# Optimization experiments

Hardware: AMD Instinct MI355X
Metric: run time of the kernel (lower is better)

The kernel has to match this reference:

```python
import jax, jax.numpy as jnp
import numpy as np

N0, N1, N2, N3 = 8192, 32768, 65536, 65536
CUM = (N0, N0 + N1, N0 + N1 + N2, N0 + N1 + N2 + N3)  # nodes through hop k
NTOT = CUM[3]
EH = (131072, 262144, 262144)                          # edges per hop (per edge type)
ECUM = (EH[0], EH[0] + EH[1], EH[0] + EH[1] + EH[2])
ETOT = ECUM[2]
C, H, T = 64, 256, 3
HH = H // 2
B, L = 16, 512  # N0 == B * L: equal-length note sequences per graph
LN_EPS = 1e-5


def _ln(x, w, b):
    m = x.mean(-1, keepdims=True)
    v = x.var(-1, keepdims=True)
    return (x - m) / jnp.sqrt(v + LN_EPS) * w + b


def _seg_mean(msgs, dst, n):
    s = jax.ops.segment_sum(msgs, dst, num_segments=n)
    cnt = jax.ops.segment_sum(jnp.ones(dst.shape, msgs.dtype), dst, num_segments=n)
    return s / jnp.maximum(cnt, 1.0)[:, None]


def _l2(x):
    return x / jnp.maximum(jnp.linalg.norm(x, axis=-1, keepdims=True), 1e-12)


def _gru_dir(x, wih, whh, bih, bhh, reverse):
    # x: [B, Lt, Din]; torch gate order (r, z, n)
    gi = jnp.einsum('bld,gd->blg', x, wih) + bih
    gi = jnp.moveaxis(gi, 1, 0)  # [Lt, B, 3*HH]
    h0 = jnp.zeros((x.shape[0], HH), x.dtype)

    def step(h, g):
        gh = h @ whh.T + bhh
        ir, iz, in_ = jnp.split(g, 3, -1)
        hr, hz, hn = jnp.split(gh, 3, -1)
        r = jax.nn.sigmoid(ir + hr)
        z = jax.nn.sigmoid(iz + hz)
        n = jnp.tanh(in_ + r * hn)
        hnew = (1.0 - z) * n + z * h
        return hnew, hnew

    _, ys = jax.lax.scan(step, h0, gi, reverse=reverse)
    return jnp.moveaxis(ys, 0, 1)  # [B, Lt, HH]


def _bigru(x, wih, whh, bih, bhh):
    f = _gru_dir(x, wih[0], whh[0], bih[0], bhh[0], False)
    bwd = _gru_dir(x, wih[1], whh[1], bih[1], bhh[1], True)
    return jnp.concatenate([f, bwd], -1)


def _forward(x, edge_index, batch_size, sage0_proj_w, sage0_proj_b, sage0_lw, sage0_lb,
             sage0_rw, sage_lw, sage_lb, sage_rw, ln_w, ln_b,
             gru_wih0, gru_whh0, gru_bih0, gru_bhh0,
             gru_wih1, gru_whh1, gru_bih1, gru_bhh1,
             rnn_norm_w, rnn_norm_b, mlp1_w, mlp1_b, mlp_ln_w, mlp_ln_b,
             mlp2_w, mlp2_b, cat_w, cat_b):
    # ---- hybrid GRU branch on seed notes (equal lengths -> pad == reshape) ----
    xs = x[:batch_size].reshape(B, L, C)
    h = _bigru(xs, gru_wih0, gru_whh0, gru_bih0, gru_bhh0)
    h = _bigru(h, gru_wih1, gru_whh1, gru_bih1, gru_bhh1)  # inter-layer dropout: eval mode
    h = _ln(h, rnn_norm_w, rnn_norm_b)
    h = _ln(jax.nn.relu(h @ mlp1_w + mlp1_b), mlp_ln_w, mlp_ln_b) @ mlp2_w + mlp2_b
    x_rnn = h.reshape(batch_size, H)

    # ---- GNN layer 0: SAGEConv(project=True, normalize=True), hetero mean over T types ----
    feat = x
    outs = []
    for t in range(T):
        src, dst = edge_index[t, 0], edge_index[t, 1]
        xp = jax.nn.relu(feat @ sage0_proj_w[t] + sage0_proj_b[t])
        agg = _seg_mean(xp[src], dst, NTOT)
        outs.append(_l2(agg @ sage0_lw[t] + sage0_lb[t] + feat @ sage0_rw[t]))
    feat = sum(outs) / T
    feat = _ln(jax.nn.relu(feat), ln_w[0], ln_b[0])  # dropout: eval mode (identity)

    # ---- layers 1..2 with trim_to_layer: drop last sampled hop each layer ----
    n_layer = (CUM[2], CUM[1])
    e_layer = (ECUM[1], ECUM[0])
    for i in range(2):
        n, e = n_layer[i], e_layer[i]
        feat = feat[:n]
        outs = []
        for t in range(T):
            src, dst = edge_index[t, 0, :e], edge_index[t, 1, :e]
            agg = _seg_mean(feat[src], dst, n)
            outs.append(agg @ sage_lw[i, t] + sage_lb[i, t] + feat @ sage_rw[i, t])
        feat = sum(outs) / T
        if i == 0:
            feat = _ln(jax.nn.relu(feat), ln_w[1], ln_b[1])
    x_gnn = feat[:batch_size]
    return jnp.concatenate([x_rnn, x_gnn], -1) @ cat_w + cat_b


def setup_inputs():
    key = jax.random.key(0)
    ks = iter(jax.random.split(key, 64))

    def nrm(shape, fan_in):
        return jax.random.normal(next(ks), shape, jnp.float32) / float(np.sqrt(fan_in))

    # hop-structured edges: hop k has src < CUM[k+1], dst < CUM[k]
    ei = []
    for t in range(T):
        rows, cols = [], []
        for k in range(3):
            rows.append(jax.random.randint(next(ks), (EH[k],), 0, CUM[k + 1]))
            cols.append(jax.random.randint(next(ks), (EH[k],), 0, CUM[k]))
        ei.append(jnp.stack([jnp.concatenate(rows), jnp.concatenate(cols)]))
    edge_index = jnp.stack(ei).astype(jnp.int32)

    return dict(
        x=jax.random.normal(next(ks), (NTOT, C), jnp.float32),
        edge_index=edge_index,
        batch=(jnp.arange(N0) // L).astype(jnp.int32),
        batch_size=N0,
        sage0_proj_w=nrm((T, C, C), C), sage0_proj_b=jnp.zeros((T, C), jnp.float32),
        sage0_lw=nrm((T, C, H), C), sage0_lb=jnp.zeros((T, H), jnp.float32),
        sage0_rw=nrm((T, C, H), C),
        sage_lw=nrm((2, T, H, H), H), sage_lb=jnp.zeros((2, T, H), jnp.float32),
        sage_rw=nrm((2, T, H, H), H),
        ln_w=jnp.ones((2, H), jnp.float32), ln_b=jnp.zeros((2, H), jnp.float32),
        gru_wih0=nrm((2, 3 * HH, C), C), gru_whh0=nrm((2, 3 * HH, HH), HH),
        gru_bih0=jnp.zeros((2, 3 * HH), jnp.float32), gru_bhh0=jnp.zeros((2, 3 * HH), jnp.float32),
        gru_wih1=nrm((2, 3 * HH, H), H), gru_whh1=nrm((2, 3 * HH, HH), HH),
        gru_bih1=jnp.zeros((2, 3 * HH), jnp.float32), gru_bhh1=jnp.zeros((2, 3 * HH), jnp.float32),
        rnn_norm_w=jnp.ones((H,), jnp.float32), rnn_norm_b=jnp.zeros((H,), jnp.float32),
        mlp1_w=nrm((H, H), H), mlp1_b=jnp.zeros((H,), jnp.float32),
        mlp_ln_w=jnp.ones((H,), jnp.float32), mlp_ln_b=jnp.zeros((H,), jnp.float32),
        mlp2_w=nrm((H, H), H), mlp2_b=jnp.zeros((H,), jnp.float32),
        cat_w=nrm((2 * H, H), 2 * H), cat_b=jnp.zeros((H,), jnp.float32),
    )


def reference(x, edge_index, batch, batch_size, sage0_proj_w, sage0_proj_b, sage0_lw,
              sage0_lb, sage0_rw, sage_lw, sage_lb, sage_rw, ln_w, ln_b,
              gru_wih0, gru_whh0, gru_bih0, gru_bhh0, gru_wih1, gru_whh1, gru_bih1,
              gru_bhh1, rnn_norm_w, rnn_norm_b, mlp1_w, mlp1_b, mlp_ln_w, mlp_ln_b,
              mlp2_w, mlp2_b, cat_w, cat_b):
    # batch encodes 16 equal-length (512) sequences; bincount/pad == reshape above
    return _forward(x, edge_index, batch_size, sage0_proj_w, sage0_proj_b, sage0_lw,
                    sage0_lb, sage0_rw, sage_lw, sage_lb, sage_rw, ln_w, ln_b,
                    gru_wih0, gru_whh0, gru_bih0, gru_bhh0, gru_wih1, gru_whh1,
                    gru_bih1, gru_bhh1, rnn_norm_w, rnn_norm_b, mlp1_w, mlp1_b,
                    mlp_ln_w, mlp_ln_b, mlp2_w, mlp2_b, cat_w, cat_b)
```

## Files before the change

kernel.cpp:

```cpp
#include <hip/hip_runtime.h>
#include <stdint.h>

typedef unsigned short u16;
typedef __attribute__((ext_vector_type(8))) short short8;
typedef __attribute__((ext_vector_type(4))) short short4v;
typedef __attribute__((ext_vector_type(4))) float float4v;

#define DEV static __device__ __forceinline__

DEV float bf2f(u16 u){ union { unsigned int i; float f; } c; c.i = ((unsigned int)u) << 16; return c.f; }
DEV u16 f2bf(float f){ union { float ff; unsigned int i; } c; c.ff = f;
  unsigned int x = c.i; return (u16)((x + 0x7fffu + ((x >> 16) & 1u)) >> 16); }

#define MFMA16(a,b,c) __builtin_amdgcn_mfma_f32_16x16x32_bf16((a),(b),(c),0,0,0)

#define ETOTC  655360
#define TSTRIDE 155648
#define NBINS   466944

struct SM {
  u16 As[64*72];
  u16 Bs[256*72];
  float redS[4][64];
  float redQ[4][64];
  float rowA[64], rowB[64];
};

__global__ void detect_dtype(const u16* __restrict__ xs, int* __restrict__ flag){
  __shared__ int sh[256];
  int t = threadIdx.x; int cnt = 0;
  for (int i = t; i < 4096; i += 256){
    u16 u = xs[i]; int e = (u >> 7) & 0xff;
    cnt += (u == 0 || (e >= 112 && e <= 143)) ? 1 : 0;
  }
  sh[t] = cnt; __syncthreads();
  for (int d = 128; d; d >>= 1){ if (t < d) sh[t] += sh[t+d]; __syncthreads(); }
  if (t == 0) flag[0] = (sh[0] >= 3686) ? 1 : 0;
}

DEV u16 scrub(u16 v){ int e = (v >> 7) & 0xff; return (e == 0xff) ? (u16)0 : v; }

__global__ void convert_x(const void* __restrict__ xin, const int* __restrict__ flag,
                          u16* __restrict__ out){
  int i = blockIdx.x*256 + threadIdx.x;
  u16 v[4];
  if (flag[0] == 1){
    short4v s = ((const short4v*)xin)[i];
#pragma unroll
    for (int j=0;j<4;j++) v[j] = scrub((u16)s[j]);
  } else {
    float4v f = ((const float4v*)xin)[i];
#pragma unroll
    for (int j=0;j<4;j++) v[j] = scrub(f2bf(f[j]));
  }
  short4v o; o[0]=(short)v[0]; o[1]=(short)v[1]; o[2]=(short)v[2]; o[3]=(short)v[3];
  ((short4v*)out)[i] = o;
}

struct WSrc { const void* p[28]; };
__device__ const int g_wcum[29] = {0,12288,12480,61632,62400,111552,504768,506304,899520,
  900032,900544,949696,1048000,1048768,1049536,1246144,1344448,1345216,1345984,1346240,
  1346496,1412032,1412288,1412544,1412800,1478336,1478592,1609664,1609920};

__global__ void convert_w(WSrc d, const int* __restrict__ flag, u16* __restrict__ out){
  int i = blockIdx.x*256 + threadIdx.x;
  if (i >= 1609920) return;
  int lo = 0, hi = 28;
  while (hi - lo > 1){ int m = (lo+hi) >> 1; if (i >= g_wcum[m]) lo = m; else hi = m; }
  int off = i - g_wcum[lo];
  u16 v = (flag[0] == 1) ? ((const u16*)d.p[lo])[off]
                         : f2bf(((const float*)d.p[lo])[off]);
  out[i] = scrub(v);
}

__global__ void packT(const u16* __restrict__ in, u16* __restrict__ out, int K, int N){
  int i = blockIdx.x*256 + threadIdx.x;
  if (i < K*N){ int n = i / K, k = i - n*K; out[i] = in[(size_t)k*N + n]; }
}

__global__ void pack_lr(const u16* __restrict__ lw, const u16* __restrict__ rw,
                        u16* __restrict__ out, int F){
  int K2 = 2*F; long total = 3L*256*K2;
  long i = (long)blockIdx.x*256 + threadIdx.x;
  if (i < total){
    int k = (int)(i % K2); int n = (int)((i / K2) & 255); int t = (int)(i / ((long)K2*256));
    out[i] = (k < F) ? lw[((size_t)t*F + k)*256 + n]
                     : rw[((size_t)t*F + (k-F))*256 + n];
  }
}

__global__ void hist3(const int* __restrict__ ei, int* __restrict__ cnt){
  int g = blockIdx.x*256 + threadIdx.x;
  int t = g / ETOTC, e = g - t*ETOTC;
  int dst = ei[(size_t)t*2*ETOTC + ETOTC + e];
  int base = t*TSTRIDE;
  atomicAdd(&cnt[base + dst], 1);
  if (e < 393216) atomicAdd(&cnt[base + 106496 + dst], 1);
  if (e < 131072) atomicAdd(&cnt[base + 147456 + dst], 1);
}

__global__ void perm3(const int* __restrict__ ei, const int* __restrict__ off,
                      int* __restrict__ slot, int* __restrict__ srcs){
  int g = blockIdx.x*256 + threadIdx.x;
  int t = g / ETOTC, e = g - t*ETOTC;
  int dst = ei[(size_t)t*2*ETOTC + ETOTC + e];
  int src = ei[(size_t)t*2*ETOTC + e];
  int base = t*TSTRIDE;
  { int b = base + dst; srcs[off[b] + atomicAdd(&slot[b], 1)] = src; }
  if (e < 393216){ int b = base + 106496 + dst;
    srcs[off[b] + atomicAdd(&slot[b], 1)] = src; }
  if (e < 131072){ int b = base + 147456 + dst;
    srcs[off[b] + atomicAdd(&slot[b], 1)] = src; }
}

__global__ void scan_blocks(const int* __restrict__ cnt, int* __restrict__ off,
                            int* __restrict__ bsum, int n){
  __shared__ int sh[256];
  int t = threadIdx.x;
  int base = blockIdx.x*2048 + t*8;
  int v[8]; int tot = 0;
#pragma unroll
  for (int j=0;j<8;j++){ v[j] = (base+j < n) ? cnt[base+j] : 0; tot += v[j]; }
  sh[t] = tot; __syncthreads();
  for (int d=1; d<256; d<<=1){
    int y = (t>=d) ? sh[t-d] : 0; __syncthreads();
    sh[t] += y; __syncthreads();
  }
  int run = sh[t] - tot;
#pragma unroll
  for (int j=0;j<8;j++){ if (base+j < n) off[base+j] = run; run += v[j]; }
  if (t == 255) bsum[blockIdx.x] = sh[255];
}

__global__ void scan_top(int* __restrict__ bsum, int G){
  __shared__ int sh[256];
  int t = threadIdx.x;
  int v = (t < G) ? bsum[t] : 0;
  sh[t] = v; __syncthreads();
  for (int d=1; d<256; d<<=1){
    int y = (t>=d) ? sh[t-d] : 0; __syncthreads();
    sh[t] += y; __syncthreads();
  }
  if (t < G) bsum[t] = sh[t] - v;
}

__global__ void scan_add(int* __restrict__ off, const int* __restrict__ bsum, int n){
  int add = bsum[blockIdx.x];
  int base = blockIdx.x*2048 + threadIdx.x*8;
#pragma unroll
  for (int j=0;j<8;j++) if (base+j < n) off[base+j] += add;
}

template<int F>
DEV void gather_body(int w, int lane,
    const int* __restrict__ off, const int* __restrict__ cnt, const int* __restrict__ srcs,
    const u16* __restrict__ feat, int ld, u16* __restrict__ out)
{
  int st = off[w], c = cnt[w];
  float sc = 1.f / (float)(c < 1 ? 1 : c);
  if (F == 64) {
    float a = 0.f, b = 0.f;
    int i = 0;
    for (; i + 4 <= c; i += 4){
      int s0 = srcs[st+i], s1 = srcs[st+i+1], s2 = srcs[st+i+2], s3 = srcs[st+i+3];
      u16 u0 = feat[(size_t)s0*ld + lane];
      u16 u1 = feat[(size_t)s1*ld + lane];
      u16 u2 = feat[(size_t)s2*ld + lane];
      u16 u3 = feat[(size_t)s3*ld + lane];
      a += bf2f(u0) + bf2f(u1);
      b += bf2f(u2) + bf2f(u3);
    }
    for (; i < c; ++i){ int s = srcs[st+i]; a += bf2f(feat[(size_t)s*ld + lane]); }
    out[(size_t)w*64 + lane] = f2bf((a + b)*sc);
  } else {
    float a0=0.f,a1=0.f,a2=0.f,a3=0.f;
    float b0=0.f,b1=0.f,b2=0.f,b3=0.f;
    int i = 0;
    for (; i + 4 <= c; i += 4){
      int s0 = srcs[st+i], s1 = srcs[st+i+1], s2 = srcs[st+i+2], s3 = srcs[st+i+3];
      short4v u0 = *(const short4v*)(feat + (size_t)s0*ld + lane*4);
      short4v u1 = *(const short4v*)(feat + (size_t)s1*ld + lane*4);
      short4v u2 = *(const short4v*)(feat + (size_t)s2*ld + lane*4);
      short4v u3 = *(const short4v*)(feat + (size_t)s3*ld + lane*4);
      a0 += bf2f((u16)u0[0]) + bf2f((u16)u1[0]);
      a1 += bf2f((u16)u0[1]) + bf2f((u16)u1[1]);
      a2 += bf2f((u16)u0[2]) + bf2f((u16)u1[2]);
      a3 += bf2f((u16)u0[3]) + bf2f((u16)u1[3]);
      b0 += bf2f((u16)u2[0]) + bf2f((u16)u3[0]);
      b1 += bf2f((u16)u2[1]) + bf2f((u16)u3[1]);
      b2 += bf2f((u16)u2[2]) + bf2f((u16)u3[2]);
      b3 += bf2f((u16)u2[3]) + bf2f((u16)u3[3]);
    }
    for (; i < c; ++i){
      int s = srcs[st+i];
      short4v u = *(const short4v*)(feat + (size_t)s*ld + lane*4);
      a0 += bf2f((u16)u[0]); a1 += bf2f((u16)u[1]);
      a2 += bf2f((u16)u[2]); a3 += bf2f((u16)u[3]);
    }
    u16* o = out + (size_t)w*256 + lane*4;
    o[0]=f2bf((a0+b0)*sc); o[1]=f2bf((a1+b1)*sc);
    o[2]=f2bf((a2+b2)*sc); o[3]=f2bf((a3+b3)*sc);
  }
}

DEV void ln_body(int r, int lane,
    const u16* __restrict__ in, u16* __restrict__ out,
    const u16* __restrict__ w, const u16* __restrict__ b)
{
  short4v u = *(const short4v*)(in + (size_t)r*256 + lane*4);
  float v[4];
#pragma unroll
  for (int i=0;i<4;i++) v[i] = bf2f((u16)u[i]);
  float s = v[0]+v[1]+v[2]+v[3];
  float q = v[0]*v[0]+v[1]*v[1]+v[2]*v[2]+v[3]*v[3];
#pragma unroll
  for (int d=1; d<64; d<<=1){ s += __shfl_xor(s, d); q += __shfl_xor(q, d); }
  float mu = s * (1.f/256.f);
  float var = fmaxf(q * (1.f/256.f) - mu*mu, 0.f);
  float rs = rsqrtf(var + 1e-5f);
  u16* o = out + (size_t)r*256 + lane*4;
#pragma unroll
  for (int i=0;i<4;i++){
    int col = lane*4 + i;
    o[i] = f2bf((v[i]-mu)*rs*bf2f(w[col]) + bf2f(b[col]));
  }
}

#define LGKM0_SB do{ asm volatile("s_waitcnt lgkmcnt(0)" ::: "memory"); \
                     __builtin_amdgcn_sched_barrier(0); \
                     __builtin_amdgcn_s_barrier(); \
                     __builtin_amdgcn_sched_barrier(0); }while(0)

#define GRU_STEP(S, C0, C1, C2) do{                                          \
    const int l_ = dir ? (511 - (S)) : (S);                                  \
    short8 afr_[4];                                                          \
    _Pragma("unroll")                                                        \
    for (int kt=0; kt<4; kt++) afr_[kt] = *(const short8*)(&hbf[kt*32 + lg*8]); \
    float4v acc_[4];                                                         \
    _Pragma("unroll")                                                        \
    for (int nt=0; nt<4; nt++) acc_[nt] = (float4v){0.f,0.f,0.f,0.f};        \
    _Pragma("unroll")                                                        \
    for (int kt=0; kt<4; kt++){                                              \
      _Pragma("unroll")                                                      \
      for (int nt=0; nt<4; nt++) acc_[nt] = MFMA16(afr_[kt], bfrag[nt][kt], acc_[nt]); } \
    if (lane < 16){                                                          \
      _Pragma("unroll")                                                      \
      for (int nt=0; nt<4; nt++) ghs[64*w + nt*16 + lane] = acc_[nt][0];     \
    }                                                                        \
    LGKM0_SB;                                                                \
    if (tid < 128){                                                          \
      float ghr = ghs[tid]       + bhr;                                      \
      float ghz = ghs[128 + tid] + bhz;                                      \
      float ghn = ghs[256 + tid] + bhn;                                      \
      float r_ = 1.f/(1.f + __expf(-((C0) + ghr)));                          \
      float z_ = 1.f/(1.f + __expf(-((C1) + ghz)));                          \
      float xn_ = (C2) + r_*ghn;                                             \
      float th_ = 1.f - 2.f/(__expf(2.f*xn_) + 1.f);                         \
      hreg = (1.f - z_)*th_ + z_*hreg;                                       \
      u16 hb_ = f2bf(hreg);                                                  \
      hbf[tid] = hb_;                                                        \
      hout[((size_t)(b*512 + l_))*256 + dir*128 + tid] = hb_;                \
      int sn_ = (S) + 2;                                                     \
      if (sn_ < 512){                                                        \
        int ln2_ = dir ? (511 - sn_) : sn_;                                  \
        const float* g_ = gbase + (size_t)ln2_*768;                          \
        (C0) = g_[0]; (C1) = g_[128]; (C2) = g_[256];                        \
      }                                                                      \
    }                                                                        \
    LGKM0_SB;                                                                \
  }while(0)

DEV void gru_body(const float* __restrict__ gi, const u16* __restrict__ whh,
                  const u16* __restrict__ bhh, u16* __restrict__ hout,
                  int bid, u16* hbf, float* ghs)
{
  const int b = bid >> 1, dir = bid & 1;
  const int tid = threadIdx.x;
  const int w = tid >> 6, lane = tid & 63;
  const int lr = lane & 15, lg = lane >> 4;

  short8 bfrag[4][4];
#pragma unroll
  for (int nt=0; nt<4; nt++)
#pragma unroll
    for (int kt=0; kt<4; kt++){
      int n = 64*w + nt*16 + lr;
      bfrag[nt][kt] = *(const short8*)(whh + ((size_t)(dir*384 + n))*128 + kt*32 + lg*8);
    }

  const float* gbase = gi + (size_t)b*512*768 + dir*384 + tid;
  float hreg = 0.f, bhr = 0.f, bhz = 0.f, bhn = 0.f;
  float a0=0.f,a1=0.f,a2=0.f, e0=0.f,e1=0.f,e2=0.f;
  if (tid < 128){
    bhr = bf2f(bhh[dir*384 + tid]);
    bhz = bf2f(bhh[dir*384 + 128 + tid]);
    bhn = bf2f(bhh[dir*384 + 256 + tid]);
    const float* g0 = gbase + (size_t)(dir ? 511 : 0)*768;
    a0 = g0[0]; a1 = g0[128]; a2 = g0[256];
    const float* g1 = gbase + (size_t)(dir ? 510 : 1)*768;
    e0 = g1[0]; e1 = g1[128]; e2 = g1[256];
  }
  if (tid < 64) ((unsigned int*)hbf)[tid] = 0u;
  LGKM0_SB;

  __builtin_amdgcn_s_setprio(1);
  for (int s2 = 0; s2 < 512; s2 += 2){
    GRU_STEP(s2,     a0, a1, a2);
    GRU_STEP(s2 + 1, e0, e1, e2);
  }
  __builtin_amdgcn_s_setprio(0);
}

template<int F>
__global__ __launch_bounds__(384,1) void fused_gru_gather(
    const float* __restrict__ gi, const u16* __restrict__ whh,
    const u16* __restrict__ bhh, u16* __restrict__ hout,
    const int* __restrict__ off0, const int* __restrict__ cnt0, const int* __restrict__ srcs,
    const u16* __restrict__ feat, int ld, int featstep,
    u16* __restrict__ aggout, long aggstride, int rows, int bpt)
{
  __shared__ u16 hbf[128];
  __shared__ float ghs[384];
  if (blockIdx.x < 32){
    gru_body(gi, whh, bhh, hout, blockIdx.x, hbf, ghs);
    return;
  }
  int gb = blockIdx.x - 32;
  int t = gb / bpt, rb = gb - t*bpt;
  int w = rb*6 + (threadIdx.x >> 6);
  int lane = threadIdx.x & 63;
  if (w >= rows) return;
  gather_body<F>(w, lane, off0 + t*TSTRIDE, cnt0 + t*TSTRIDE, srcs,
                 feat + (size_t)t*featstep, ld, aggout + (size_t)t*aggstride);
}

template<int EPI, bool OUTF32>
DEV void gemm_body(SM& sm, int bx, int by,
    const u16* __restrict__ A, int lda,
    const u16* __restrict__ WT, int K, int N,
    const u16* __restrict__ bias,
    const u16* __restrict__ lnw, const u16* __restrict__ lnb,
    void* __restrict__ Cp, int ldc, const int* __restrict__ dynof)
{
  u16* As = sm.As; u16* Bs = sm.Bs;
  const int tid = threadIdx.x;
  const int lane = tid & 63, wid = tid >> 6;
  const int lr = lane & 15, lg = lane >> 4;
  const int m0 = bx * 64;
  const int col0 = by * 256;
  float4v acc[4][4];
#pragma unroll
  for (int i=0;i<4;i++)
#pragma unroll
    for (int j=0;j<4;j++) acc[i][j] = (float4v){0.f,0.f,0.f,0.f};

  for (int k0 = 0; k0 < K; k0 += 64){
#pragma unroll
    for (int v = 0; v < 2; v++){
      int idx = tid + v*256; int r = idx >> 3, c8 = (idx & 7) << 3;
      *(short8*)(&As[r*72 + c8]) = *(const short8*)(A + (size_t)(m0+r)*lda + k0 + c8);
    }
#pragma unroll
    for (int v = 0; v < 8; v++){
      int idx = tid + v*256; int nn = idx >> 3, c8 = (idx & 7) << 3;
      short8 val = {0,0,0,0,0,0,0,0};
      if (col0 + nn < N) val = *(const short8*)(WT + (size_t)(col0+nn)*K + k0 + c8);
      *(short8*)(&Bs[nn*72 + c8]) = val;
    }
    __syncthreads();
#pragma unroll
    for (int kk = 0; kk < 2; kk++){
      short8 af[4], bfr[4];
#pragma unroll
      for (int i=0;i<4;i++) af[i]  = *(const short8*)(&As[(16*i+lr)*72 + kk*32 + lg*8]);
#pragma unroll
      for (int j=0;j<4;j++) bfr[j] = *(const short8*)(&Bs[(wid*64+16*j+lr)*72 + kk*32 + lg*8]);
#pragma unroll
      for (int i=0;i<4;i++)
#pragma unroll
        for (int j=0;j<4;j++) acc[i][j] = MFMA16(af[i], bfr[j], acc[i][j]);
    }
    __syncthreads();
  }
  int cols[4];
#pragma unroll
  for (int j=0;j<4;j++) cols[j] = col0 + wid*64 + 16*j + lr;
#pragma unroll
  for (int j=0;j<4;j++){
    float bv = (cols[j] < N) ? bf2f(bias[cols[j]]) : 0.f;
#pragma unroll
    for (int i=0;i<4;i++)
#pragma unroll
      for (int r=0;r<4;r++) acc[i][j][r] += bv;
  }
  if (EPI >= 1){
#pragma unroll
    for (int i=0;i<4;i++)
#pragma unroll
      for (int j=0;j<4;j++)
#pragma unroll
        for (int r=0;r<4;r++) acc[i][j][r] = fmaxf(acc[i][j][r], 0.f);
  }
  if (EPI == 2){
#pragma unroll
    for (int i=0;i<4;i++)
#pragma unroll
      for (int r=0;r<4;r++){
        float p = acc[i][0][r]+acc[i][1][r]+acc[i][2][r]+acc[i][3][r];
        float q = acc[i][0][r]*acc[i][0][r]+acc[i][1][r]*acc[i][1][r]
                 +acc[i][2][r]*acc[i][2][r]+acc[i][3][r]*acc[i][3][r];
#pragma unroll
        for (int d=1; d<16; d<<=1){ p += __shfl_xor(p,d); q += __shfl_xor(q,d); }
        if (lr == 0){ sm.redS[wid][16*i + lg*4 + r] = p; sm.redQ[wid][16*i + lg*4 + r] = q; }
      }
    __syncthreads();
    if (tid < 64){
      float s = sm.redS[0][tid]+sm.redS[1][tid]+sm.redS[2][tid]+sm.redS[3][tid];
      float q = sm.redQ[0][tid]+sm.redQ[1][tid]+sm.redQ[2][tid]+sm.redQ[3][tid];
      float mu = s * (1.f/256.f);
      float var = fmaxf(q * (1.f/256.f) - mu*mu, 0.f);
      sm.rowA[tid] = mu; sm.rowB[tid] = rsqrtf(var + 1e-5f);
    }
    __syncthreads();
#pragma unroll
    for (int i=0;i<4;i++)
#pragma unroll
      for (int r=0;r<4;r++){
        int rl = 16*i + lg*4 + r;
        float mu = sm.rowA[rl], rs = sm.rowB[rl];
#pragma unroll
        for (int j=0;j<4;j++){
          float w = bf2f(lnw[cols[j]]), bb = bf2f(lnb[cols[j]]);
          acc[i][j][r] = (acc[i][j][r]-mu)*rs*w + bb;
        }
      }
  }
  bool of32 = OUTF32;
  if (dynof) of32 = (dynof[0] == 0);
#pragma unroll
  for (int i=0;i<4;i++)
#pragma unroll
    for (int r=0;r<4;r++){
      int row = m0 + 16*i + lg*4 + r;
#pragma unroll
      for (int j=0;j<4;j++) if (cols[j] < N){
        if (of32) ((float*)Cp)[(size_t)row*ldc + cols[j]] = acc[i][j][r];
        else ((u16*)Cp)[(size_t)row*ldc + cols[j]] = f2bf(acc[i][j][r]);
      }
    }
}

template<int EPI, bool OUTF32>
__global__ __launch_bounds__(256,1) void gemm_bt(
    const u16* __restrict__ A, int lda,
    const u16* __restrict__ WT, int K, int N,
    const u16* __restrict__ bias,
    const u16* __restrict__ lnw, const u16* __restrict__ lnb,
    void* __restrict__ Cp, int ldc, const int* __restrict__ dynof)
{
  __shared__ SM sm;
  gemm_body<EPI,OUTF32>(sm, blockIdx.x, blockIdx.y, A, lda, WT, K, N, bias, lnw, lnb, Cp, ldc, dynof);
}

template<int F, bool DO_L2, bool DO_LN>
DEV void sage_body(SM& sm, int bx,
    const u16* __restrict__ A1, long a1t, const u16* __restrict__ A2, int lda2,
    const u16* __restrict__ WTp, const u16* __restrict__ lbp,
    const u16* __restrict__ lnw, const u16* __restrict__ lnb,
    u16* __restrict__ out, int ldc, int outcol)
{
  constexpr int K2 = 2*F;
  u16* As = sm.As; u16* Bs = sm.Bs;
  const int tid = threadIdx.x;
  const int lane = tid & 63, wid = tid >> 6;
  const int lr = lane & 15, lg = lane >> 4;
  const int m0 = bx * 64;
  int colsL[4];
#pragma unroll
  for (int j=0;j<4;j++) colsL[j] = wid*64 + 16*j + lr;
  float4v facc[4][4];
#pragma unroll
  for (int i=0;i<4;i++)
#pragma unroll
    for (int j=0;j<4;j++) facc[i][j] = (float4v){0.f,0.f,0.f,0.f};

  for (int t=0; t<3; ++t){
    float4v acc[4][4];
#pragma unroll
    for (int i=0;i<4;i++)
#pragma unroll
      for (int j=0;j<4;j++) acc[i][j] = (float4v){0.f,0.f,0.f,0.f};
    const u16* WT  = WTp + (size_t)t*256*K2;
    const u16* A1b = A1 + (size_t)t*a1t;
    for (int k0 = 0; k0 < K2; k0 += 64){
      const u16* Ab; int la, kb;
      if (k0 < F){ Ab = A1b; la = F; kb = k0; } else { Ab = A2; la = lda2; kb = k0 - F; }
#pragma unroll
      for (int v=0; v<2; v++){
        int idx = tid + v*256; int r = idx >> 3, c8 = (idx & 7) << 3;
        *(short8*)(&As[r*72 + c8]) = *(const short8*)(Ab + (size_t)(m0+r)*la + kb + c8);
      }
#pragma unroll
      for (int v=0; v<8; v++){
        int idx = tid + v*256; int nn = idx >> 3, c8 = (idx & 7) << 3;
        *(short8*)(&Bs[nn*72 + c8]) = *(const short8*)(WT + (size_t)nn*K2 + k0 + c8);
      }
      __syncthreads();
#pragma unroll
      for (int kk = 0; kk < 2; kk++){
        short8 af[4], bfr[4];
#pragma unroll
        for (int i=0;i<4;i++) af[i]  = *(const short8*)(&As[(16*i+lr)*72 + kk*32 + lg*8]);
#pragma unroll
        for (int j=0;j<4;j++) bfr[j] = *(const short8*)(&Bs[(wid*64+16*j+lr)*72 + kk*32 + lg*8]);
#pragma unroll
        for (int i=0;i<4;i++)
#pragma unroll
          for (int j=0;j<4;j++) acc[i][j] = MFMA16(af[i], bfr[j], acc[i][j]);
      }
      __syncthreads();
    }
#pragma unroll
    for (int j=0;j<4;j++){
      float bv = bf2f(lbp[t*256 + colsL[j]]);
#pragma unroll
      for (int i=0;i<4;i++)
#pragma unroll
        for (int r=0;r<4;r++) acc[i][j][r] += bv;
    }
    if (DO_L2){
#pragma unroll
      for (int i=0;i<4;i++)
#pragma unroll
        for (int r=0;r<4;r++){
          float q = acc[i][0][r]*acc[i][0][r]+acc[i][1][r]*acc[i][1][r]
                   +acc[i][2][r]*acc[i][2][r]+acc[i][3][r]*acc[i][3][r];
#pragma unroll
          for (int d=1; d<16; d<<=1) q += __shfl_xor(q,d);
          if (lr == 0) sm.redQ[wid][16*i + lg*4 + r] = q;
        }
      __syncthreads();
      if (tid < 64){
        float q = sm.redQ[0][tid]+sm.redQ[1][tid]+sm.redQ[2][tid]+sm.redQ[3][tid];
        sm.rowA[tid] = 1.f / fmaxf(sqrtf(q), 1e-12f);
      }
      __syncthreads();
#pragma unroll
      for (int i=0;i<4;i++)
#pragma unroll
        for (int r=0;r<4;r++){
          float sc = sm.rowA[16*i + lg*4 + r];
#pragma unroll
          for (int j=0;j<4;j++) acc[i][j][r] *= sc;
        }
      __syncthreads();
    }
#pragma unroll
    for (int i=0;i<4;i++)
#pragma unroll
      for (int j=0;j<4;j++)
#pragma unroll
        for (int r=0;r<4;r++) facc[i][j][r] += acc[i][j][r];
  }
  const float inv3 = (1.f/3.f);
#pragma unroll
  for (int i=0;i<4;i++)
#pragma unroll
    for (int j=0;j<4;j++)
#pragma unroll
      for (int r=0;r<4;r++) facc[i][j][r] *= inv3;
  if (DO_LN){
#pragma unroll
    for (int i=0;i<4;i++)
#pragma unroll
      for (int j=0;j<4;j++)
#pragma unroll
        for (int r=0;r<4;r++) facc[i][j][r] = fmaxf(facc[i][j][r], 0.f);
#pragma unroll
    for (int i=0;i<4;i++)
#pragma unroll
      for (int r=0;r<4;r++){
        float p = facc[i][0][r]+facc[i][1][r]+facc[i][2][r]+facc[i][3][r];
        float q = facc[i][0][r]*facc[i][0][r]+facc[i][1][r]*facc[i][1][r]
                 +facc[i][2][r]*facc[i][2][r]+facc[i][3][r]*facc[i][3][r];
#pragma unroll
        for (int d=1; d<16; d<<=1){ p += __shfl_xor(p,d); q += __shfl_xor(q,d); }
        if (lr == 0){ sm.redS[wid][16*i + lg*4 + r] = p; sm.redQ[wid][16*i + lg*4 + r] = q; }
      }
    __syncthreads();
    if (tid < 64){
      float s = sm.redS[0][tid]+sm.redS[1][tid]+sm.redS[2][tid]+sm.redS[3][tid];
      float q = sm.redQ[0][tid]+sm.redQ[1][tid]+sm.redQ[2][tid]+sm.redQ[3][tid];
      float mu = s * (1.f/256.f);
      float var = fmaxf(q * (1.f/256.f) - mu*mu, 0.f);
      sm.rowA[tid] = mu; sm.rowB[tid] = rsqrtf(var + 1e-5f);
    }
    __syncthreads();
#pragma unroll
    for (int i=0;i<4;i++)
#pragma unroll
      for (int r=0;r<4;r++){
        int rl = 16*i + lg*4 + r;
        float mu = sm.rowA[rl], rs = sm.rowB[rl];
#pragma unroll
        for (int j=0;j<4;j++){
          float w = bf2f(lnw[colsL[j]]), bb = bf2f(lnb[colsL[j]]);
          facc[i][j][r] = (facc[i][j][r]-mu)*rs*w + bb;
        }
      }
  }
#pragma unroll
  for (int i=0;i<4;i++)
#pragma unroll
    for (int r=0;r<4;r++){
      int row = m0 + 16*i + lg*4 + r;
#pragma unroll
      for (int j=0;j<4;j++)
        out[(size_t)row*ldc + outcol + colsL[j]] = f2bf(facc[i][j][r]);
    }
}

__global__ __launch_bounds__(256,1) void fused_gemm_sage0(
    const u16* __restrict__ H0, const u16* __restrict__ wih1b, const u16* __restrict__ bih1b,
    float* __restrict__ GI,
    const u16* __restrict__ AGGB0, const u16* __restrict__ x16, const u16* __restrict__ WP0,
    const u16* __restrict__ s0lb, const u16* __restrict__ lnw, const u16* __restrict__ lnb,
    u16* __restrict__ FEAT)
{
  __shared__ SM sm;
  int b = blockIdx.x;
  if (b < 384)
    gemm_body<0,true>(sm, b & 127, b >> 7, H0, 256, wih1b, 256, 768, bih1b,
                      nullptr, nullptr, GI, 768, nullptr);
  else
    sage_body<64,true,true>(sm, b - 384, AGGB0, (long)106496*64, x16, 64, WP0, s0lb,
                            lnw, lnb, FEAT, 256, 0);
}

__global__ __launch_bounds__(256,1) void fused_ln_sage1(
    const u16* __restrict__ AGGB1, const u16* __restrict__ FEAT, const u16* __restrict__ WP1,
    const u16* __restrict__ slb, const u16* __restrict__ lnw, const u16* __restrict__ lnb,
    u16* __restrict__ FEAT2,
    const u16* __restrict__ H1, u16* __restrict__ HA,
    const u16* __restrict__ rnw, const u16* __restrict__ rnb)
{
  __shared__ SM sm;
  int b = blockIdx.x;
  if (b < 640)
    sage_body<256,false,true>(sm, b, AGGB1, (long)40960*256, FEAT, 256, WP1, slb,
                              lnw, lnb, FEAT2, 256, 0);
  else {
    int r = (b - 640)*4 + (threadIdx.x >> 6);
    ln_body(r, threadIdx.x & 63, H1, HA, rnw, rnb);
  }
}

__global__ __launch_bounds__(256,1) void fused_mlp1_gather2(
    const u16* __restrict__ HA, const u16* __restrict__ M1T, const u16* __restrict__ mlp1b,
    const u16* __restrict__ mlnw, const u16* __restrict__ mlnb, u16* __restrict__ HB,
    const int* __restrict__ OFF, const int* __restrict__ CNT, const int* __restrict__ SRCS,
    const u16* __restrict__ FEAT2, u16* __restrict__ AGGB2)
{
  __shared__ SM sm;
  int b = blockIdx.x;
  if (b < 128){
    gemm_body<2,false>(sm, b, 0, HA, 256, M1T, 256, 256, mlp1b, mlnw, mlnb, HB, 256, nullptr);
  } else {
    int g = b - 128;
    int t = g / 2048, rb = g - t*2048;
    int w = rb*4 + (threadIdx.x >> 6);
    int lane = threadIdx.x & 63;
    if (w < 8192)
      gather_body<256>(w, lane, OFF + t*TSTRIDE + 147456, CNT + t*TSTRIDE + 147456, SRCS,
                       FEAT2, 256, AGGB2 + (size_t)t*8192*256);
  }
}

__global__ __launch_bounds__(256,1) void fused_mlp2_sage2(
    const u16* __restrict__ HB, const u16* __restrict__ M2T, const u16* __restrict__ mlp2b,
    u16* __restrict__ CAT,
    const u16* __restrict__ AGGB2, const u16* __restrict__ FEAT2, const u16* __restrict__ WP2,
    const u16* __restrict__ slb2)
{
  __shared__ SM sm;
  int b = blockIdx.x;
  if (b < 128)
    gemm_body<0,false>(sm, b, 0, HB, 256, M2T, 256, 256, mlp2b, nullptr, nullptr, CAT, 512, nullptr);
  else
    sage_body<256,false,false>(sm, b - 128, AGGB2, (long)8192*256, FEAT2, 256, WP2, slb2,
                               nullptr, nullptr, CAT, 512, 256);
}

extern "C" void kernel_launch(void* const* d_in, const int* in_sizes, int n_in,
                              void* d_out, int out_size, void* d_ws, size_t ws_size,
                              hipStream_t stream)
{
  (void)in_sizes; (void)n_in; (void)out_size;
  const int* ei = (const int*)d_in[1];

  char* ws = (char*)d_ws;
  size_t o = 0;
  auto alloc = [&](size_t b){ size_t p = o; o += (b + 255) & ~(size_t)255; return p; };
  char* RA   = ws + alloc(66060288);
  u16* XP3   = (u16*)RA;
  u16* AGGB1 = (u16*)RA;
  char* RR   = ws + alloc(41943040);
  float* GI  = (float*)RR;
  u16* H0    = (u16*)(RR + 25165824);
  u16* H1    = (u16*)(RR + 29360128);
  u16* HA    = (u16*)(RR + 33554432);
  u16* HB    = (u16*)(RR + 37748736);
  char* RB   = ws + alloc(40894464);
  u16* AGGB0 = (u16*)RB;
  u16* AGGB2 = (u16*)RB;
  u16* FEAT2 = (u16*)(RB + 12582912);
  u16* FEAT  = (u16*)(ws + alloc(106496ull*256*2));
  u16* CAT   = (u16*)(ws + alloc(8192ull*512*2));
  u16* AR    = (u16*)(ws + alloc(12619968ull*2));
  u16* WXP   = (u16*)(ws + alloc(192ull*64*2));
  u16* WP0   = (u16*)(ws + alloc(3ull*256*128*2));
  u16* WP1   = (u16*)(ws + alloc(3ull*256*512*2));
  u16* WP2   = (u16*)(ws + alloc(3ull*256*512*2));
  u16* M1T   = (u16*)(ws + alloc(256ull*256*2));
  u16* M2T   = (u16*)(ws + alloc(256ull*256*2));
  u16* CTT   = (u16*)(ws + alloc(256ull*512*2));
  int* CNT   = (int*)(ws + alloc((size_t)NBINS*4));
  int* OFF   = (int*)(ws + alloc((size_t)NBINS*4));
  int* SLOT  = (int*)(ws + alloc((size_t)NBINS*4));
  int* BSUM  = (int*)(ws + alloc(256ull*4));
  int* SRCS  = (int*)(ws + alloc(3538944ull*4));
  int* FLAG  = (int*)(ws + alloc(256));
  if (o > ws_size) return;

  u16* x16    = AR;
  u16* projw6 = AR + 11010048; u16* projb6 = AR + 11022336;
  u16* s0lw6  = AR + 11022528; u16* s0lb6  = AR + 11071680; u16* s0rw6 = AR + 11072448;
  u16* slw6   = AR + 11121600; u16* slb6   = AR + 11514816; u16* srw6  = AR + 11516352;
  u16* lnw6   = AR + 11909568; u16* lnb6   = AR + 11910080;
  u16* wih0b  = AR + 11910592; u16* whh0b  = AR + 11959744;
  u16* bih0b  = AR + 12058048; u16* bhh0b  = AR + 12058816;
  u16* wih1b  = AR + 12059584; u16* whh1b  = AR + 12256192;
  u16* bih1b  = AR + 12354496; u16* bhh1b  = AR + 12355264;
  u16* rnw6   = AR + 12356032; u16* rnb6   = AR + 12356288;
  u16* mlp1w6 = AR + 12356544; u16* mlp1b6 = AR + 12422080;
  u16* mlnw6  = AR + 12422336; u16* mlnb6  = AR + 12422592;
  u16* mlp2w6 = AR + 12422848; u16* mlp2b6 = AR + 12488384;
  u16* catw6  = AR + 12488640; u16* catb6  = AR + 12619712;

  detect_dtype<<<dim3(1),dim3(256),0,stream>>>((const u16*)d_in[0], FLAG);
  convert_x<<<dim3(10752),dim3(256),0,stream>>>(d_in[0], FLAG, x16);
  WSrc wsrc;
  for (int i=0;i<28;i++) wsrc.p[i] = d_in[4+i];
  convert_w<<<dim3(6289),dim3(256),0,stream>>>(wsrc, FLAG, AR + 11010048);

  packT<<<dim3(256),dim3(256),0,stream>>>(mlp1w6, M1T, 256, 256);
  packT<<<dim3(256),dim3(256),0,stream>>>(mlp2w6, M2T, 256, 256);
  packT<<<dim3(512),dim3(256),0,stream>>>(catw6,  CTT, 512, 256);
  for (int t=0;t<3;t++)
    packT<<<dim3(16),dim3(256),0,stream>>>(projw6 + (size_t)t*4096, WXP + (size_t)t*4096, 64, 64);
  pack_lr<<<dim3(384),dim3(256),0,stream>>>(s0lw6, s0rw6, WP0, 64);
  pack_lr<<<dim3(1536),dim3(256),0,stream>>>(slw6,               srw6,               WP1, 256);
  pack_lr<<<dim3(1536),dim3(256),0,stream>>>(slw6 + 3ull*256*256, srw6 + 3ull*256*256, WP2, 256);

  hipMemsetAsync(CNT, 0, (size_t)NBINS*4, stream);
  hist3<<<dim3(7680),dim3(256),0,stream>>>(ei, CNT);
  scan_blocks<<<dim3(228),dim3(256),0,stream>>>(CNT, OFF, BSUM, NBINS);
  scan_top<<<dim3(1),dim3(256),0,stream>>>(BSUM, 228);
  scan_add<<<dim3(228),dim3(256),0,stream>>>(OFF, BSUM, NBINS);
  hipMemsetAsync(SLOT, 0, (size_t)NBINS*4, stream);
  perm3<<<dim3(7680),dim3(256),0,stream>>>(ei, OFF, SLOT, SRCS);

  gemm_bt<0,true><<<dim3(128,3),dim3(256),0,stream>>>(x16, 64, wih0b, 64, 768, bih0b, nullptr, nullptr, GI, 768, nullptr);
  gemm_bt<1,false><<<dim3(2688,1),dim3(256),0,stream>>>(x16, 64, WXP, 64, 192, projb6, nullptr, nullptr, XP3, 192, nullptr);

  fused_gru_gather<64><<<dim3(32 + 3*17750),dim3(384),0,stream>>>(
      GI, whh0b, bhh0b, H0,
      OFF, CNT, SRCS, XP3, 192, 64, AGGB0, (long)106496*64, 106496, 17750);

  fused_gemm_sage0<<<dim3(2048),dim3(256),0,stream>>>(
      H0, wih1b, bih1b, GI,
      AGGB0, x16, WP0, s0lb6, lnw6, lnb6, FEAT);

  fused_gru_gather<256><<<dim3(32 + 3*6827),dim3(384),0,stream>>>(
      GI, whh1b, bhh1b, H1,
      OFF + 106496, CNT + 106496, SRCS, FEAT, 256, 0, AGGB1, (long)40960*256, 40960, 6827);

  fused_ln_sage1<<<dim3(2688),dim3(256),0,stream>>>(
      AGGB1, FEAT, WP1, slb6, lnw6+256, lnb6+256, FEAT2,
      H1, HA, rnw6, rnb6);

  fused_mlp1_gather2<<<dim3(6272),dim3(256),0,stream>>>(
      HA, M1T, mlp1b6, mlnw6, mlnb6, HB,
      OFF, CNT, SRCS, FEAT2, AGGB2);

  fused_mlp2_sage2<<<dim3(256),dim3(256),0,stream>>>(
      HB, M2T, mlp2b6, CAT,
      AGGB2, FEAT2, WP2, slb6 + 3*256);

  gemm_bt<0,false><<<dim3(128,1),dim3(256),0,stream>>>(CAT, 512, CTT, 512, 256, catb6,
      nullptr, nullptr, d_out, 256, FLAG);
}
```

Baseline: 1.586 ms.

## Fuse histogram/permutation passes with input GEMMs and drop GRU priority boost

Merges the edge histogram kernel with the first GRU input-projection GEMM, and the edge permutation kernel with the x-projection GEMM. Each pair now runs as one launch that dispatches on block index. This lets compute-bound and atomic-bound blocks share the GPU concurrently and cuts launch count. Both memsets are moved earlier, and the s_setprio boost around the GRU recurrence loop is removed, which may change how that serial loop competes with gather blocks for issue slots.

Result: faster. 1.539 ms (-2.9%).

```diff
diff --git a/kernel.cpp b/kernel.cpp
--- a/kernel.cpp
+++ b/kernel.cpp
@@ -89,8 +89,8 @@
   }
 }
 
-__global__ void hist3(const int* __restrict__ ei, int* __restrict__ cnt){
-  int g = blockIdx.x*256 + threadIdx.x;
+DEV void hist_body(int gb, const int* __restrict__ ei, int* __restrict__ cnt){
+  int g = gb*256 + threadIdx.x;
   int t = g / ETOTC, e = g - t*ETOTC;
   int dst = ei[(size_t)t*2*ETOTC + ETOTC + e];
   int base = t*TSTRIDE;
@@ -99,9 +99,9 @@
   if (e < 131072) atomicAdd(&cnt[base + 147456 + dst], 1);
 }
 
-__global__ void perm3(const int* __restrict__ ei, const int* __restrict__ off,
-                      int* __restrict__ slot, int* __restrict__ srcs){
-  int g = blockIdx.x*256 + threadIdx.x;
+DEV void perm_body(int gb, const int* __restrict__ ei, const int* __restrict__ off,
+                   int* __restrict__ slot, int* __restrict__ srcs){
+  int g = gb*256 + threadIdx.x;
   int t = g / ETOTC, e = g - t*ETOTC;
   int dst = ei[(size_t)t*2*ETOTC + ETOTC + e];
   int src = ei[(size_t)t*2*ETOTC + e];
@@ -303,12 +303,10 @@
   if (tid < 64) ((unsigned int*)hbf)[tid] = 0u;
   LGKM0_SB;
 
-  __builtin_amdgcn_s_setprio(1);
   for (int s2 = 0; s2 < 512; s2 += 2){
     GRU_STEP(s2,     a0, a1, a2);
     GRU_STEP(s2 + 1, e0, e1, e2);
   }
-  __builtin_amdgcn_s_setprio(0);
 }
 
 template<int F>
@@ -618,6 +616,34 @@
       for (int j=0;j<4;j++)
         out[(size_t)row*ldc + outcol + colsL[j]] = f2bf(facc[i][j][r]);
     }
+}
+
+__global__ __launch_bounds__(256,1) void fused_wih0_hist(
+    const u16* __restrict__ x16, const u16* __restrict__ wih0b, const u16* __restrict__ bih0b,
+    float* __restrict__ GI, const int* __restrict__ ei, int* __restrict__ CNT)
+{
+  __shared__ SM sm;
+  int b = blockIdx.x;
+  if (b < 384)
+    gemm_body<0,true>(sm, b & 127, b >> 7, x16, 64, wih0b, 64, 768, bih0b,
+                      nullptr, nullptr, GI, 768, nullptr);
+  else
+    hist_body(b - 384, ei, CNT);
+}
+
+__global__ __launch_bounds__(256,1) void fused_xp_perm(
+    const u16* __restrict__ x16, const u16* __restrict__ WXP, const u16* __restrict__ projb,
+    u16* __restrict__ XP3,
+    const int* __restrict__ ei, const int* __restrict__ OFF,
+    int* __restrict__ SLOT, int* __restrict__ SRCS)
+{
+  __shared__ SM sm;
+  int b = blockIdx.x;
+  if (b < 2688)
+    gemm_body<1,false>(sm, b, 0, x16, 64, WXP, 64, 192, projb,
+                       nullptr, nullptr, XP3, 192, nullptr);
+  else
+    perm_body(b - 2688, ei, OFF, SLOT, SRCS);
 }
 
 __global__ __launch_bounds__(256,1) void fused_gemm_sage0(
@@ -753,6 +779,8 @@
   for (int i=0;i<28;i++) wsrc.p[i] = d_in[4+i];
   convert_w<<<dim3(6289),dim3(256),0,stream>>>(wsrc, FLAG, AR + 11010048);
 
+  hipMemsetAsync(CNT, 0, (size_t)NBINS*4, stream);
+  hipMemsetAsync(SLOT, 0, (size_t)NBINS*4, stream);
   packT<<<dim3(256),dim3(256),0,stream>>>(mlp1w6, M1T, 256, 256);
   packT<<<dim3(256),dim3(256),0,stream>>>(mlp2w6, M2T, 256, 256);
   packT<<<dim3(512),dim3(256),0,stream>>>(catw6,  CTT, 512, 256);
@@ -762,16 +790,15 @@
   pack_lr<<<dim3(1536),dim3(256),0,stream>>>(slw6,               srw6,               WP1, 256);
   pack_lr<<<dim3(1536),dim3(256),0,stream>>>(slw6 + 3ull*256*256, srw6 + 3ull*256*256, WP2, 256);
 
-  hipMemsetAsync(CNT, 0, (size_t)NBINS*4, stream);
-  hist3<<<dim3(7680),dim3(256),0,stream>>>(ei, CNT);
+  fused_wih0_hist<<<dim3(384 + 7680),dim3(256),0,stream>>>(
+      x16, wih0b, bih0b, GI, ei, CNT);
+
   scan_blocks<<<dim3(228),dim3(256),0,stream>>>(CNT, OFF, BSUM, NBINS);
   scan_top<<<dim3(1),dim3(256),0,stream>>>(BSUM, 228);
   scan_add<<<dim3(228),dim3(256),0,stream>>>(OFF, BSUM, NBINS);
-  hipMemsetAsync(SLOT, 0, (size_t)NBINS*4, stream);
-  perm3<<<dim3(7680),dim3(256),0,stream>>>(ei, OFF, SLOT, SRCS);
-
-  gemm_bt<0,true><<<dim3(128,3),dim3(256),0,stream>>>(x16, 64, wih0b, 64, 768, bih0b, nullptr, nullptr, GI, 768, nullptr);
-  gemm_bt<1,false><<<dim3(2688,1),dim3(256),0,stream>>>(x16, 64, WXP, 64, 192, projb6, nullptr, nullptr, XP3, 192, nullptr);
+
+  fused_xp_perm<<<dim3(2688 + 7680),dim3(256),0,stream>>>(
+      x16, WXP, projb6, XP3, ei, OFF, SLOT, SRCS);
 
   fused_gru_gather<64><<<dim3(32 + 3*17750),dim3(384),0,stream>>>(
       GI, whh0b, bhh0b, H0,
```
